# Kernel tuning notes

Measured on AMD Instinct MI355X. Metric: run time of the kernel, lower is better.

The kernel has to match this reference:

```python
import jax, jax.numpy as jnp
import numpy as np

N_EMBD = 768
BLOCK_SIZE = 2048
ATTN_SPAN = 128
LN_EPS = 1e-5


def _band_mask(T, span):
    # mask[i, j] = 1 iff 0 <= i - j < span  (causal sliding window incl. diagonal)
    i = jnp.arange(T)[:, None]
    j = jnp.arange(T)[None, :]
    d = i - j
    return ((d >= 0) & (d < span)).astype(jnp.float32)


def setup_inputs() -> dict:
    key = jax.random.key(0)
    k1, k2, k3 = jax.random.split(key, 3)
    B, T, D = 8, BLOCK_SIZE, N_EMBD
    x = jax.random.normal(k1, (B, T, D), dtype=jnp.float32)
    W_qkv = jax.random.normal(k2, (D, 3 * D), dtype=jnp.float32) * (1.0 / np.sqrt(D))
    b_qkv = jax.random.normal(k3, (3 * D,), dtype=jnp.float32) * 0.02
    ln_w = jnp.ones((D,), dtype=jnp.float32)
    ln_b = jnp.zeros((D,), dtype=jnp.float32)
    return {"x": x, "W_qkv": W_qkv, "b_qkv": b_qkv, "ln_w": ln_w, "ln_b": ln_b}


def _layer_norm(h, w, b):
    mu = jnp.mean(h, axis=-1, keepdims=True)
    var = jnp.mean(jnp.square(h - mu), axis=-1, keepdims=True)
    return (h - mu) * jax.lax.rsqrt(var + LN_EPS) * w + b


def reference(x, W_qkv, b_qkv, ln_w, ln_b):
    B, T, D = x.shape
    qkv = x @ W_qkv + b_qkv                      # [B, T, 3D]
    q, k, v = jnp.split(qkv, 3, axis=-1)         # each [B, T, D]
    scale = jnp.float32(1.0 / np.sqrt(N_EMBD * ATTN_SPAN))
    scores = jnp.einsum('bid,bjd->bij', q, k) * scale   # [B, T, T]
    mask = _band_mask(T, ATTN_SPAN)              # [T, T]
    scores = scores * mask                       # zero outside sliding window
    out = jnp.einsum('bij,bjd->bid', scores, v)  # [B, T, D]
    return _layer_norm(out, ln_w, ln_b)
```

## Files before the change

kernel.cpp:

```cpp
#include <hip/hip_runtime.h>
#include <cstdint>
#include <cstddef>

typedef __attribute__((ext_vector_type(8))) short bf16x8;
typedef __attribute__((ext_vector_type(4))) float f32x4;
typedef __attribute__((ext_vector_type(8))) unsigned short u16x8;
typedef __attribute__((ext_vector_type(4))) unsigned short u16x4;

#define NB 8
#define NT 2048
#define ND 768
#define NC 2304
#define NM (NB*NT)
#define SPAN 128

__device__ __forceinline__ unsigned short f2bf(float f) {
    unsigned int u = __builtin_bit_cast(unsigned int, f);
    u += 0x7fffu + ((u >> 16) & 1u);
    return (unsigned short)(u >> 16);
}

#define GLOAD16(G, L) __builtin_amdgcn_global_load_lds( \
    (const __attribute__((address_space(1))) unsigned int*)(G), \
    (__attribute__((address_space(3))) unsigned int*)(L), 16, 0, 0)

__global__ void k_conv_x(const float* __restrict__ x, unsigned short* __restrict__ xb) {
    int i = blockIdx.x * 256 + threadIdx.x;
    const float4* p = (const float4*)x + (size_t)i * 2;
    float4 a = p[0], b = p[1];
    u16x8 v;
    v[0] = f2bf(a.x); v[1] = f2bf(a.y); v[2] = f2bf(a.z); v[3] = f2bf(a.w);
    v[4] = f2bf(b.x); v[5] = f2bf(b.y); v[6] = f2bf(b.z); v[7] = f2bf(b.w);
    *((u16x8*)xb + i) = v;
}

__global__ void k_conv_wT(const float* __restrict__ W, unsigned short* __restrict__ wT) {
    __shared__ unsigned short tile[64][72];
    const int k0 = blockIdx.x * 64, n0 = blockIdx.y * 64;
    const int tid = threadIdx.x;
    for (int e = 0; e < 16; ++e) {
        int idx = e * 256 + tid;
        int r = idx >> 6, c = idx & 63;
        tile[r][c] = f2bf(W[(size_t)(k0 + r) * NC + n0 + c]);
    }
    __syncthreads();
    for (int e = 0; e < 16; ++e) {
        int idx = e * 256 + tid;
        int r = idx & 63, c = idx >> 6;
        wT[(size_t)(n0 + c) * ND + k0 + r] = tile[r][c];
    }
}

__global__ void k_gemm(const unsigned short* __restrict__ xb,
                       const unsigned short* __restrict__ wT,
                       const float* __restrict__ bq,
                       unsigned short* __restrict__ qb,
                       unsigned short* __restrict__ kb,
                       unsigned short* __restrict__ vT) {
    __shared__ char lds[32768];
    unsigned short* Asw = (unsigned short*)lds;
    unsigned short* Bsw = (unsigned short*)(lds + 16384);
    const int tid = threadIdx.x;
    const int lane = tid & 63, w = tid >> 6;
    const int m0 = blockIdx.x * 128, n0 = blockIdx.y * 128;
    const int wr = (w >> 1) * 64, wc = (w & 1) * 64;

    f32x4 acc[4][4];
    const f32x4 zf = {0.f, 0.f, 0.f, 0.f};
#pragma unroll
    for (int i = 0; i < 4; ++i)
#pragma unroll
        for (int j = 0; j < 4; ++j) acc[i][j] = zf;

    for (int kc = 0; kc < 12; ++kc) {
        if (kc) __syncthreads();
#pragma unroll
        for (int t = 0; t < 4; ++t) {
            int chunk = w * 4 + t;
            int p = chunk * 1024 + lane * 16;
            int row = p >> 7;
            int col = (p & 127) ^ ((row & 7) << 4);
            GLOAD16(xb + (size_t)(m0 + row) * ND + kc * 64 + (col >> 1), Asw + chunk * 512);
            GLOAD16(wT + (size_t)(n0 + row) * ND + kc * 64 + (col >> 1), Bsw + chunk * 512);
        }
        __syncthreads();
#pragma unroll
        for (int kk = 0; kk < 2; ++kk) {
            bf16x8 af[4], bg[4];
#pragma unroll
            for (int i = 0; i < 4; ++i) {
                int r = wr + i * 16 + (lane & 15);
                af[i] = *(const bf16x8*)((const char*)Asw + r * 128 +
                        ((kk * 64 + (lane >> 4) * 16) ^ ((r & 7) << 4)));
                int c = wc + i * 16 + (lane & 15);
                bg[i] = *(const bf16x8*)((const char*)Bsw + c * 128 +
                        ((kk * 64 + (lane >> 4) * 16) ^ ((c & 7) << 4)));
            }
#pragma unroll
            for (int i = 0; i < 4; ++i)
#pragma unroll
                for (int j = 0; j < 4; ++j)
                    acc[i][j] = __builtin_amdgcn_mfma_f32_16x16x32_bf16(af[i], bg[j], acc[i][j], 0, 0, 0);
        }
    }

    const int third = n0 / ND;
    if (third < 2) {
        unsigned short* ob = third == 0 ? qb : kb;
        const int nl0 = n0 - third * ND + wc;
#pragma unroll
        for (int j = 0; j < 4; ++j) {
            int nl = nl0 + j * 16 + (lane & 15);
            float bias = bq[third * ND + nl];
#pragma unroll
            for (int i = 0; i < 4; ++i) {
#pragma unroll
                for (int r = 0; r < 4; ++r) {
                    int m = m0 + wr + i * 16 + (lane >> 4) * 4 + r;
                    ob[(size_t)m * ND + nl] = f2bf(acc[i][j][r] + bias);
                }
            }
        }
    } else {
        const int bb = m0 >> 11, t0g = m0 & 2047;
        const int d0 = n0 - 2 * ND;
        unsigned short* vTb = vT + ((size_t)bb * ND + d0) * NT;
        float bias[4];
#pragma unroll
        for (int j = 0; j < 4; ++j) bias[j] = bq[2 * ND + d0 + wc + j * 16 + (lane & 15)];
        unsigned short* T = (unsigned short*)lds;
        for (int h = 0; h < 2; ++h) {
            __syncthreads();
            if ((w & 1) == h) {
#pragma unroll
                for (int i = 0; i < 4; ++i)
#pragma unroll
                    for (int j = 0; j < 4; ++j) {
                        int d_loc = j * 16 + (lane & 15);
                        int t_loc = wr + i * 16 + (lane >> 4) * 4;
                        u16x4 pk;
#pragma unroll
                        for (int r = 0; r < 4; ++r) pk[r] = f2bf(acc[i][j][r] + bias[j]);
                        *(u16x4*)(T + d_loc * 136 + t_loc) = pk;
                    }
            }
            __syncthreads();
#pragma unroll
            for (int e = 0; e < 4; ++e) {
                int slot = e * 256 + tid;
                int dd = slot >> 4, ch = slot & 15;
                u16x8 v = *(const u16x8*)(T + dd * 136 + ch * 8);
                *(u16x8*)(vTb + (size_t)(h * 64 + dd) * NT + t0g + ch * 8) = v;
            }
        }
    }
}

__global__ __launch_bounds__(1024) void k_attn(const unsigned short* __restrict__ qb,
                       const unsigned short* __restrict__ kb,
                       const unsigned short* __restrict__ vT,
                       const float* __restrict__ lnw,
                       const float* __restrict__ lnb,
                       float* __restrict__ out) {
    __shared__ char smem[123904];
    unsigned short* S = (unsigned short*)smem;
    char* R = smem + 25600;

    const int tid = threadIdx.x, lane = tid & 63, w = tid >> 6;
    const int bid = blockIdx.x;
    const int nid = (bid & 7) * 32 + (bid >> 3);
    const int b = nid >> 5;
    const int q0 = (nid & 31) * 64;
    const size_t rowQ = (size_t)b * NT + q0;
    const size_t rowK = (size_t)b * NT;
    const size_t vbase = (size_t)b * ND * NT;

    f32x4 sacc[3];
    const f32x4 zf = {0.f, 0.f, 0.f, 0.f};
#pragma unroll
    for (int s = 0; s < 3; ++s) sacc[s] = zf;

    const int qrow = (w >> 2) * 16 + (lane & 15);
    const int kct = (w & 3) * 3;

    auto stage_qk = [&](int dc, int cur) {
        char* L = R + cur * 32768;
#pragma unroll
        for (int e = 0; e < 2; ++e) {
            int s = w * 128 + e * 64 + lane;
            const unsigned short* src;
            if (s < 512) {
                int r = s >> 3, sl = s & 7;
                src = qb + (rowQ + r) * ND + dc * 64 + 8 * (sl ^ (r & 7));
            } else {
                int t = s - 512;
                int r = t >> 3, sl = t & 7;
                int j = q0 - 128 + r; if (j < 0) j = 0;
                src = kb + (rowK + j) * ND + dc * 64 + 8 * (sl ^ (r & 7));
            }
            GLOAD16(src, L + (w * 128 + e * 64) * 16);
        }
    };

    stage_qk(0, 0);
    __syncthreads();
    for (int dc = 0; dc < 12; ++dc) {
        int cur = dc & 1;
        if (dc < 11) stage_qk(dc + 1, cur ^ 1);
        const char* Lq = R + cur * 32768;
        const char* Lk = Lq + 8192;
#pragma unroll
        for (int kk = 0; kk < 2; ++kk) {
            int bq_ = (((lane >> 4) * 16 + kk * 64)) ^ ((qrow & 7) << 4);
            bf16x8 aq = *(const bf16x8*)(Lq + qrow * 128 + bq_);
#pragma unroll
            for (int s = 0; s < 3; ++s) {
                int krow = (kct + s) * 16 + (lane & 15);
                int bk_ = (((lane >> 4) * 16 + kk * 64)) ^ ((krow & 7) << 4);
                bf16x8 bk = *(const bf16x8*)(Lk + krow * 128 + bk_);
                sacc[s] = __builtin_amdgcn_mfma_f32_16x16x32_bf16(aq, bk, sacc[s], 0, 0, 0);
            }
        }
        __syncthreads();
    }

    const float scl = 0.0031894436f;
#pragma unroll
    for (int s = 0; s < 3; ++s) {
        int jl = (kct + s) * 16 + (lane & 15);
        int j = q0 - 128 + jl;
#pragma unroll
        for (int e = 0; e < 4; ++e) {
            int il = (w >> 2) * 16 + (lane >> 4) * 4 + e;
            int d = (q0 + il) - j;
            float v = (d >= 0 && d < SPAN && j >= 0) ? sacc[s][e] * scl : 0.0f;
            S[il * 200 + jl] = f2bf(v);
        }
    }

    auto stage_v = [&](int c, int cur) {
        char* L = R + cur * 49152;
        int j0 = q0 - 128 + c * 32;
#pragma unroll
        for (int e = 0; e < 3; ++e) {
            int s = w * 192 + e * 64 + lane;
            int d = s >> 2, sl = s & 3;
            int j = j0 + 8 * (sl ^ (d & 3)); if (j < 0) j = 0;
            GLOAD16(vT + vbase + (size_t)d * NT + j, L + (w * 192 + e * 64) * 16);
        }
    };

    f32x4 acc[4][3];
#pragma unroll
    for (int rt = 0; rt < 4; ++rt)
#pragma unroll
        for (int ct = 0; ct < 3; ++ct) acc[rt][ct] = zf;

    stage_v(0, 0);
    __syncthreads();
    for (int c = 0; c < 6; ++c) {
        int cur = c & 1;
        if (c < 5) stage_v(c + 1, cur ^ 1);
        const char* Lv = R + cur * 49152;
        bf16x8 as[4], bv[3];
#pragma unroll
        for (int rt = 0; rt < 4; ++rt)
            as[rt] = *(const bf16x8*)((const char*)S + (rt * 16 + (lane & 15)) * 400 + c * 64 + (lane >> 4) * 16);
#pragma unroll
        for (int ct = 0; ct < 3; ++ct) {
            int d = (w * 3 + ct) * 16 + (lane & 15);
            bv[ct] = *(const bf16x8*)(Lv + d * 64 + (((lane >> 4) * 16) ^ ((d & 3) << 4)));
        }
#pragma unroll
        for (int rt = 0; rt < 4; ++rt)
#pragma unroll
            for (int ct = 0; ct < 3; ++ct)
                acc[rt][ct] = __builtin_amdgcn_mfma_f32_16x16x32_bf16(as[rt], bv[ct], acc[rt][ct], 0, 0, 0);
        __syncthreads();
    }

    float psum[4][4], pssq[4][4];
#pragma unroll
    for (int rt = 0; rt < 4; ++rt)
#pragma unroll
        for (int e = 0; e < 4; ++e) {
            float s = 0.f, q = 0.f;
#pragma unroll
            for (int ct = 0; ct < 3; ++ct) { float v = acc[rt][ct][e]; s += v; q += v * v; }
            psum[rt][e] = s; pssq[rt][e] = q;
        }
#pragma unroll
    for (int mx = 1; mx < 16; mx <<= 1)
#pragma unroll
        for (int rt = 0; rt < 4; ++rt)
#pragma unroll
            for (int e = 0; e < 4; ++e) {
                psum[rt][e] += __shfl_xor(psum[rt][e], mx, 64);
                pssq[rt][e] += __shfl_xor(pssq[rt][e], mx, 64);
            }

    float* P = (float*)R;
    float* F = (float*)(R + 8192);
    if ((lane & 15) == 0) {
#pragma unroll
        for (int rt = 0; rt < 4; ++rt)
#pragma unroll
            for (int e = 0; e < 4; ++e) {
                int r = rt * 16 + (lane >> 4) * 4 + e;
                P[(r * 16 + w) * 2] = psum[rt][e];
                P[(r * 16 + w) * 2 + 1] = pssq[rt][e];
            }
    }
    __syncthreads();
    if (tid < 64) {
        float s = 0.f, q = 0.f;
#pragma unroll
        for (int ww = 0; ww < 16; ++ww) { s += P[(tid * 16 + ww) * 2]; q += P[(tid * 16 + ww) * 2 + 1]; }
        float mu = s * (1.0f / 768.0f);
        float var = q * (1.0f / 768.0f) - mu * mu;
        F[tid * 2] = mu;
        F[tid * 2 + 1] = rsqrtf(var + 1e-5f);
    }
    __syncthreads();

    float lw[3], lb_[3];
#pragma unroll
    for (int ct = 0; ct < 3; ++ct) {
        int dcol = (w * 3 + ct) * 16 + (lane & 15);
        lw[ct] = lnw[dcol]; lb_[ct] = lnb[dcol];
    }
#pragma unroll
    for (int rt = 0; rt < 4; ++rt)
#pragma unroll
        for (int e = 0; e < 4; ++e) {
            int row = rt * 16 + (lane >> 4) * 4 + e;
            float mu = F[row * 2], rs = F[row * 2 + 1];
            float* rowp = out + (rowQ + row) * ND;
#pragma unroll
            for (int ct = 0; ct < 3; ++ct) {
                int dcol = (w * 3 + ct) * 16 + (lane & 15);
                rowp[dcol] = (acc[rt][ct][e] - mu) * rs * lw[ct] + lb_[ct];
            }
        }
}

extern "C" void kernel_launch(void* const* d_in, const int* in_sizes, int n_in,
                              void* d_out, int out_size, void* d_ws, size_t ws_size,
                              hipStream_t stream) {
    const float* x   = (const float*)d_in[0];
    const float* W   = (const float*)d_in[1];
    const float* bqv = (const float*)d_in[2];
    const float* lnw = (const float*)d_in[3];
    const float* lnb = (const float*)d_in[4];
    float* out = (float*)d_out;

    char* ws = (char*)d_ws;
    const size_t SZ_XB = (size_t)NM * ND * 2;
    const size_t SZ_WT = (size_t)NC * ND * 2;
    const size_t SZ_P  = (size_t)NM * ND * 2;
    unsigned short* xb = (unsigned short*)ws;
    unsigned short* wT = (unsigned short*)(ws + SZ_XB);
    unsigned short* qb = (unsigned short*)(ws + SZ_XB + SZ_WT);
    unsigned short* kb = (unsigned short*)(ws + SZ_XB + SZ_WT + SZ_P);
    unsigned short* vT = (unsigned short*)(ws + SZ_XB + SZ_WT + 2 * SZ_P);

    k_conv_x<<<dim3(NM * ND / (256 * 8)), dim3(256), 0, stream>>>(x, xb);
    k_conv_wT<<<dim3(ND / 64, NC / 64), dim3(256), 0, stream>>>(W, wT);
    k_gemm<<<dim3(NM / 128, NC / 128), dim3(256), 0, stream>>>(xb, wT, bqv, qb, kb, vT);
    k_attn<<<dim3(256), dim3(1024), 0, stream>>>(qb, kb, vT, lnw, lnb, out);
}
```

Measured before the change: 117.8 us.

## Fuse x fp32-to-bf16 conversion into GEMM tile load; relax attn barriers with vmcnt waits

Drops the separate x conversion kernel and its bf16 workspace. The GEMM now reads fp32 x directly, converts it in registers and writes the swizzled bf16 tile to LDS. In the attention kernel, full __syncthreads is replaced by explicit s_waitcnt vmcnt(N) plus raw s_barrier, so the next stage's async loads can stay in flight while the current buffer is consumed. The trade-off is that each GEMM block (18 column blocks per row block) re-reads and re-converts fp32 x, doubling A-side traffic through synchronous loads that no longer use the direct-to-LDS path.

Result: slower. 151.7 us (+28.7%).

```diff
diff --git a/kernel.cpp b/kernel.cpp
--- a/kernel.cpp
+++ b/kernel.cpp
@@ -23,16 +23,6 @@
 #define GLOAD16(G, L) __builtin_amdgcn_global_load_lds( \
     (const __attribute__((address_space(1))) unsigned int*)(G), \
     (__attribute__((address_space(3))) unsigned int*)(L), 16, 0, 0)
-
-__global__ void k_conv_x(const float* __restrict__ x, unsigned short* __restrict__ xb) {
-    int i = blockIdx.x * 256 + threadIdx.x;
-    const float4* p = (const float4*)x + (size_t)i * 2;
-    float4 a = p[0], b = p[1];
-    u16x8 v;
-    v[0] = f2bf(a.x); v[1] = f2bf(a.y); v[2] = f2bf(a.z); v[3] = f2bf(a.w);
-    v[4] = f2bf(b.x); v[5] = f2bf(b.y); v[6] = f2bf(b.z); v[7] = f2bf(b.w);
-    *((u16x8*)xb + i) = v;
-}
 
 __global__ void k_conv_wT(const float* __restrict__ W, unsigned short* __restrict__ wT) {
     __shared__ unsigned short tile[64][72];
@@ -51,7 +41,7 @@
     }
 }
 
-__global__ void k_gemm(const unsigned short* __restrict__ xb,
+__global__ void k_gemm(const float* __restrict__ x,
                        const unsigned short* __restrict__ wT,
                        const float* __restrict__ bq,
                        unsigned short* __restrict__ qb,
@@ -80,8 +70,18 @@
             int p = chunk * 1024 + lane * 16;
             int row = p >> 7;
             int col = (p & 127) ^ ((row & 7) << 4);
-            GLOAD16(xb + (size_t)(m0 + row) * ND + kc * 64 + (col >> 1), Asw + chunk * 512);
             GLOAD16(wT + (size_t)(n0 + row) * ND + kc * 64 + (col >> 1), Bsw + chunk * 512);
+        }
+#pragma unroll
+        for (int e = 0; e < 4; ++e) {
+            int s = e * 256 + tid;
+            int row = s >> 3, sl = s & 7;
+            const float4* src = (const float4*)(x + (size_t)(m0 + row) * ND + kc * 64 + sl * 8);
+            float4 a = src[0], b = src[1];
+            u16x8 v;
+            v[0] = f2bf(a.x); v[1] = f2bf(a.y); v[2] = f2bf(a.z); v[3] = f2bf(a.w);
+            v[4] = f2bf(b.x); v[5] = f2bf(b.y); v[6] = f2bf(b.z); v[7] = f2bf(b.w);
+            *(u16x8*)((char*)Asw + row * 128 + ((sl * 16) ^ ((row & 7) << 4))) = v;
         }
         __syncthreads();
 #pragma unroll
@@ -203,10 +203,15 @@
     };
 
     stage_qk(0, 0);
-    __syncthreads();
     for (int dc = 0; dc < 12; ++dc) {
         int cur = dc & 1;
-        if (dc < 11) stage_qk(dc + 1, cur ^ 1);
+        if (dc < 11) {
+            stage_qk(dc + 1, cur ^ 1);
+            asm volatile("s_waitcnt vmcnt(2)" ::: "memory");
+        } else {
+            asm volatile("s_waitcnt vmcnt(0)" ::: "memory");
+        }
+        __builtin_amdgcn_s_barrier();
         const char* Lq = R + cur * 32768;
         const char* Lk = Lq + 8192;
 #pragma unroll
@@ -221,7 +226,7 @@
                 sacc[s] = __builtin_amdgcn_mfma_f32_16x16x32_bf16(aq, bk, sacc[s], 0, 0, 0);
             }
         }
-        __syncthreads();
+        __builtin_amdgcn_s_barrier();
     }
 
     const float scl = 0.0031894436f;
@@ -237,6 +242,7 @@
             S[il * 200 + jl] = f2bf(v);
         }
     }
+    asm volatile("s_waitcnt lgkmcnt(0)" ::: "memory");
 
     auto stage_v = [&](int c, int cur) {
         char* L = R + cur * 49152;
@@ -257,10 +263,15 @@
         for (int ct = 0; ct < 3; ++ct) acc[rt][ct] = zf;
 
     stage_v(0, 0);
-    __syncthreads();
     for (int c = 0; c < 6; ++c) {
         int cur = c & 1;
-        if (c < 5) stage_v(c + 1, cur ^ 1);
+        if (c < 5) {
+            stage_v(c + 1, cur ^ 1);
+            asm volatile("s_waitcnt vmcnt(3)" ::: "memory");
+        } else {
+            asm volatile("s_waitcnt vmcnt(0)" ::: "memory");
+        }
+        __builtin_amdgcn_s_barrier();
         const char* Lv = R + cur * 49152;
         bf16x8 as[4], bv[3];
 #pragma unroll
@@ -276,7 +287,7 @@
 #pragma unroll
             for (int ct = 0; ct < 3; ++ct)
                 acc[rt][ct] = __builtin_amdgcn_mfma_f32_16x16x32_bf16(as[rt], bv[ct], acc[rt][ct], 0, 0, 0);
-        __syncthreads();
+        __builtin_amdgcn_s_barrier();
     }
 
     float psum[4][4], pssq[4][4];
@@ -358,14 +369,12 @@
     const size_t SZ_XB = (size_t)NM * ND * 2;
     const size_t SZ_WT = (size_t)NC * ND * 2;
     const size_t SZ_P  = (size_t)NM * ND * 2;
-    unsigned short* xb = (unsigned short*)ws;
     unsigned short* wT = (unsigned short*)(ws + SZ_XB);
     unsigned short* qb = (unsigned short*)(ws + SZ_XB + SZ_WT);
     unsigned short* kb = (unsigned short*)(ws + SZ_XB + SZ_WT + SZ_P);
     unsigned short* vT = (unsigned short*)(ws + SZ_XB + SZ_WT + 2 * SZ_P);
 
-    k_conv_x<<<dim3(NM * ND / (256 * 8)), dim3(256), 0, stream>>>(x, xb);
     k_conv_wT<<<dim3(ND / 64, NC / 64), dim3(256), 0, stream>>>(W, wT);
-    k_gemm<<<dim3(NM / 128, NC / 128), dim3(256), 0, stream>>>(xb, wT, bqv, qb, kb, vT);
+    k_gemm<<<dim3(NM / 128, NC / 128), dim3(256), 0, stream>>>(x, wT, bqv, qb, kb, vT);
     k_attn<<<dim3(256), dim3(1024), 0, stream>>>(qb, kb, vT, lnw, lnb, out);
 }
```
